# Kernel optimization log

Measured on AMD Instinct MI355X. Metric: run time of the kernel, lower is better.

Reference implementation:

```python
import jax, jax.numpy as jnp
import numpy as np

B, N, W, H = 2, 2048, 1024, 16
HD = W // H  # head dim = 64
STD = 0.02


def setup_inputs() -> dict:
    key = jax.random.key(0)
    ks = jax.random.split(key, 8)
    x = jax.random.normal(ks[0], (B, N, W), dtype=jnp.float32)
    # weights stored [in, out] (transposed vs torch nn.Linear)
    qkv_w = jax.random.normal(ks[1], (W, 3 * W), dtype=jnp.float32) * STD
    qkv_b = jnp.zeros((3 * W,), jnp.float32)
    proj_w = jax.random.normal(ks[2], (W, W), dtype=jnp.float32) * STD
    proj_b = jnp.zeros((W,), jnp.float32)
    fc_w = jax.random.normal(ks[3], (W, 4 * W), dtype=jnp.float32) * STD
    fc_b = jnp.zeros((4 * W,), jnp.float32)
    fc2_w = jax.random.normal(ks[4], (4 * W, W), dtype=jnp.float32) * STD
    fc2_b = jnp.zeros((W,), jnp.float32)
    ln1_g = jnp.ones((W,), jnp.float32)
    ln1_b = jnp.zeros((W,), jnp.float32)
    ln2_g = jnp.ones((W,), jnp.float32)
    ln2_b = jnp.zeros((W,), jnp.float32)
    return dict(x=x, ln1_g=ln1_g, ln1_b=ln1_b, qkv_w=qkv_w, qkv_b=qkv_b,
                proj_w=proj_w, proj_b=proj_b, ln2_g=ln2_g, ln2_b=ln2_b,
                fc_w=fc_w, fc_b=fc_b, fc2_w=fc2_w, fc2_b=fc2_b)


def _layernorm(x, g, b, eps=1e-5):
    mu = jnp.mean(x, axis=-1, keepdims=True)
    var = jnp.var(x, axis=-1, keepdims=True)
    return (x - mu) * jax.lax.rsqrt(var + eps) * g + b


def _attention(x, qkv_w, qkv_b, proj_w, proj_b):
    bs, n, w = x.shape
    qkv = x @ qkv_w + qkv_b                      # [b, n, 3W]
    qkv = qkv.reshape(bs, n, H, 3 * HD)
    q, k, v = jnp.split(qkv, 3, axis=-1)         # each [b, n, h, hd]
    scale = 1.0 / np.sqrt(np.sqrt(HD)).astype(np.float32)
    # hand-rolled attention: full [b, h, t, s] score matrix, fp32 softmax
    weight = jnp.einsum('bthc,bshc->bhts', q * scale, k * scale)
    weight = jax.nn.softmax(weight.astype(jnp.float32), axis=-1).astype(weight.dtype)
    out = jnp.einsum('bhts,bshc->bthc', weight, v).reshape(bs, n, w)
    return out @ proj_w + proj_b


def reference(x, ln1_g, ln1_b, qkv_w, qkv_b, proj_w, proj_b,
              ln2_g, ln2_b, fc_w, fc_b, fc2_w, fc2_b):
    x = x + _attention(_layernorm(x, ln1_g, ln1_b), qkv_w, qkv_b, proj_w, proj_b)
    h = _layernorm(x, ln2_g, ln2_b)
    h = jax.nn.gelu(h @ fc_w + fc_b, approximate=False) @ fc2_w + fc2_b
    return x + h
```

## Files before the change

### kernel.cpp

```cpp
#include <hip/hip_runtime.h>
#include <hip/hip_bf16.h>
#include <type_traits>
#include <cstdint>

using bf16 = __hip_bfloat16;
typedef __attribute__((ext_vector_type(8))) short bf16x8;
typedef __attribute__((ext_vector_type(4))) float f32x4;

__device__ __forceinline__ float bf2f(unsigned short u) {
    union { unsigned int i; float f; } c; c.i = ((unsigned int)u) << 16; return c.f;
}

#define GLLDS16(gp, lp)                                                          \
    __builtin_amdgcn_global_load_lds(                                            \
        (const __attribute__((address_space(1))) void*)(gp),                     \
        (__attribute__((address_space(3))) void*)(lp), 16, 0, 0)

__global__ __launch_bounds__(256) void transpose_f2b(const float* __restrict__ w,
                                                     bf16* __restrict__ wt,
                                                     int K, int N) {
    __shared__ bf16 t[32][33];
    const int tid = threadIdx.x;
    const int n0 = blockIdx.x * 32, k0 = blockIdx.y * 32;
#pragma unroll
    for (int i = 0; i < 4; ++i) {
        int idx = tid + i * 256;
        int r = idx >> 5, c = idx & 31;
        t[r][c] = __float2bfloat16(w[(size_t)(k0 + r) * N + n0 + c]);
    }
    __syncthreads();
#pragma unroll
    for (int i = 0; i < 4; ++i) {
        int idx = tid + i * 256;
        int r = idx >> 5, c = idx & 31;
        wt[(size_t)(n0 + r) * K + k0 + c] = t[c][r];
    }
}

__global__ __launch_bounds__(256) void vtrans_kernel(const bf16* __restrict__ qkv,
                                                     bf16* __restrict__ vtg) {
    __shared__ bf16 t[32][33];
    const int tid = threadIdx.x;
    const int s0 = blockIdx.x * 32, c0 = blockIdx.y * 32;
    const int bh = blockIdx.z, b = bh >> 4, h = bh & 15;
#pragma unroll
    for (int i = 0; i < 4; ++i) {
        int idx = tid + i * 256;
        int r = idx >> 5, c = idx & 31;
        t[r][c] = qkv[(size_t)(b * 2048 + s0 + r) * 3072 + h * 192 + 128 + c0 + c];
    }
    __syncthreads();
#pragma unroll
    for (int i = 0; i < 4; ++i) {
        int idx = tid + i * 256;
        int r = idx >> 5, c = idx & 31;
        vtg[((size_t)bh * 64 + c0 + r) * 2048 + s0 + c] = t[c][r];
    }
}

template <typename InT>
__global__ __launch_bounds__(256) void ln_kernel(const InT* __restrict__ x,
                                                 const float* __restrict__ g,
                                                 const float* __restrict__ bta,
                                                 bf16* __restrict__ y) {
    const int row = blockIdx.x, tid = threadIdx.x;
    const size_t base = (size_t)row * 1024 + tid * 4;
    float v[4];
    if constexpr (std::is_same_v<InT, float>) {
        float4 f = *(const float4*)(x + base);
        v[0] = f.x; v[1] = f.y; v[2] = f.z; v[3] = f.w;
    } else {
        ushort4 u = *(const ushort4*)((const unsigned short*)x + base);
        v[0] = bf2f(u.x); v[1] = bf2f(u.y); v[2] = bf2f(u.z); v[3] = bf2f(u.w);
    }
    float s = v[0] + v[1] + v[2] + v[3];
    float sq = v[0]*v[0] + v[1]*v[1] + v[2]*v[2] + v[3]*v[3];
#pragma unroll
    for (int off = 32; off > 0; off >>= 1) {
        s  += __shfl_down(s, off);
        sq += __shfl_down(sq, off);
    }
    __shared__ float red[8];
    const int wave = tid >> 6, lane = tid & 63;
    if (lane == 0) { red[wave] = s; red[4 + wave] = sq; }
    __syncthreads();
    s  = red[0] + red[1] + red[2] + red[3];
    sq = red[4] + red[5] + red[6] + red[7];
    const float mu   = s * (1.0f / 1024.0f);
    const float var  = sq * (1.0f / 1024.0f) - mu * mu;
    const float rstd = rsqrtf(var + 1e-5f);
#pragma unroll
    for (int e = 0; e < 4; ++e) {
        int col = tid * 4 + e;
        float yy = (v[e] - mu) * rstd * g[col] + bta[col];
        y[base + e] = __float2bfloat16(yy);
    }
}

template <int EPI, int BM>
__global__ __launch_bounds__(256) void gemm_kernel(const bf16* __restrict__ A,
                                                   const bf16* __restrict__ Bt,
                                                   const float* __restrict__ bias,
                                                   const void* __restrict__ resid,
                                                   void* __restrict__ Cout,
                                                   int M, int N, int K) {
    constexpr int IF = 4;
    constexpr int JF = (BM == 128) ? 4 : 2;
    __shared__ bf16 As[BM][72];
    __shared__ bf16 Bs[128][72];
    const int tid  = threadIdx.x;
    const int wave = tid >> 6, lane = tid & 63;
    const int quad = lane >> 4, l16 = lane & 15;
    const int wm = (BM == 128) ? (wave >> 1) * 64 : 0;
    const int wn = (BM == 128) ? (wave & 1) * 64 : wave * 32;
    const int bm = blockIdx.y * BM, bn = blockIdx.x * 128;

    int kz0 = 0, kz1 = K;
    if constexpr (EPI == 4) {
        kz0 = blockIdx.z * (K >> 1);
        kz1 = kz0 + (K >> 1);
    }

    f32x4 acc[IF][JF];
#pragma unroll
    for (int i = 0; i < IF; ++i)
#pragma unroll
        for (int j = 0; j < JF; ++j) acc[i][j] = (f32x4){0.f, 0.f, 0.f, 0.f};

    for (int kt = kz0; kt < kz1; kt += 64) {
        __syncthreads();
#pragma unroll
        for (int i = 0; i < BM * 8 / 256; ++i) {
            int c0 = tid + i * 256;
            int r = c0 >> 3, kc = (c0 & 7) << 3;
            *(uint4*)(&As[r][kc]) = *(const uint4*)(A + (size_t)(bm + r) * K + kt + kc);
        }
#pragma unroll
        for (int i = 0; i < 4; ++i) {
            int c0 = tid + i * 256;
            int r = c0 >> 3, kc = (c0 & 7) << 3;
            *(uint4*)(&Bs[r][kc]) = *(const uint4*)(Bt + (size_t)(bn + r) * K + kt + kc);
        }
        __syncthreads();
#pragma unroll
        for (int ks = 0; ks < 2; ++ks) {
            bf16x8 af[IF], bfr[JF];
#pragma unroll
            for (int i = 0; i < IF; ++i)
                af[i] = *(const bf16x8*)(&As[wm + i * 16 + l16][ks * 32 + quad * 8]);
#pragma unroll
            for (int j = 0; j < JF; ++j)
                bfr[j] = *(const bf16x8*)(&Bs[wn + j * 16 + l16][ks * 32 + quad * 8]);
#pragma unroll
            for (int i = 0; i < IF; ++i)
#pragma unroll
                for (int j = 0; j < JF; ++j)
                    acc[i][j] = __builtin_amdgcn_mfma_f32_16x16x32_bf16(af[i], bfr[j], acc[i][j], 0, 0, 0);
        }
    }
    float* skdst = nullptr;
    if constexpr (EPI == 4)
        skdst = blockIdx.z ? (float*)const_cast<void*>(resid) : (float*)Cout;
#pragma unroll
    for (int i = 0; i < IF; ++i) {
#pragma unroll
        for (int j = 0; j < JF; ++j) {
#pragma unroll
            for (int r = 0; r < 4; ++r) {
                const int row = bm + wm + i * 16 + quad * 4 + r;
                const int col = bn + wn + j * 16 + l16;
                float v = acc[i][j][r];
                if constexpr (EPI != 4) v += bias[col];
                if constexpr (EPI == 1)
                    v = 0.5f * v * (1.0f + erff(v * 0.70710678118654752f));
                if constexpr (EPI == 2) {
                    v += ((const float*)resid)[(size_t)row * N + col];
                    ((bf16*)Cout)[(size_t)row * N + col] = __float2bfloat16(v);
                } else if constexpr (EPI == 3) {
                    v += bf2f(((const unsigned short*)resid)[(size_t)row * N + col]);
                    ((float*)Cout)[(size_t)row * N + col] = v;
                } else if constexpr (EPI == 4) {
                    skdst[(size_t)row * N + col] = v;
                } else {
                    ((bf16*)Cout)[(size_t)row * N + col] = __float2bfloat16(v);
                }
            }
        }
    }
}

__global__ __launch_bounds__(256) void merge_fc2(const float* __restrict__ p0,
                                                 const float* __restrict__ p1,
                                                 const float* __restrict__ bias,
                                                 const bf16* __restrict__ resid,
                                                 float* __restrict__ outp) {
    const int idx = blockIdx.x * 256 + threadIdx.x;
    const int row = idx >> 8, col = (idx & 255) * 4;
    const size_t off = (size_t)row * 1024 + col;
    float4 a = *(const float4*)(p0 + off);
    float4 b = *(const float4*)(p1 + off);
    float4 bs = *(const float4*)(bias + col);
    ushort4 r = *(const ushort4*)((const unsigned short*)resid + off);
    float4 o;
    o.x = a.x + b.x + bs.x + bf2f(r.x);
    o.y = a.y + b.y + bs.y + bf2f(r.y);
    o.z = a.z + b.z + bs.z + bf2f(r.z);
    o.w = a.w + b.w + bs.w + bf2f(r.w);
    *(float4*)(outp + off) = o;
}

__global__ __launch_bounds__(256) void attn_kernel(const bf16* __restrict__ qkv,
                                                   const bf16* __restrict__ vtg,
                                                   bf16* __restrict__ Opart,
                                                   float* __restrict__ Lp) {
    __shared__ __align__(16) bf16 Ks[64 * 64];
    __shared__ __align__(16) bf16 Vs[64 * 64];
    __shared__ __align__(16) bf16 Ps[4][2][16][72];
    const int tid  = threadIdx.x;
    const int wave = tid >> 6, lane = tid & 63;
    const int quad = lane >> 4, l16 = lane & 15;
    const int qt = blockIdx.x, h = blockIdx.y;
    const int b = blockIdx.z >> 1, seg = blockIdx.z & 1;
    const size_t tok0 = (size_t)b * 2048;
    const int qbase = qt * 128 + wave * 32;

    bf16x8 qf[2][2];
#pragma unroll
    for (int set = 0; set < 2; ++set) {
        const bf16* qp = qkv + (tok0 + qbase + set * 16 + l16) * 3072 + h * 192 + quad * 8;
        qf[set][0] = *(const bf16x8*)(qp);
        qf[set][1] = *(const bf16x8*)(qp + 32);
    }

    const int swc = ((tid & 7) ^ ((tid >> 3) & 7)) * 8;
    const bf16* kg = qkv + (tok0 + (tid >> 3)) * 3072 + h * 192 + 64 + swc;
    const bf16* vg = vtg + ((size_t)(b * 16 + h) * 64 + (tid >> 3)) * 2048 + swc;

    const short oneb = 0x3f80;
    const bf16x8 ones = {oneb, oneb, oneb, oneb, oneb, oneb, oneb, oneb};

    f32x4 o[2][4], l_acc[2];
#pragma unroll
    for (int set = 0; set < 2; ++set) {
        l_acc[set] = (f32x4){0.f, 0.f, 0.f, 0.f};
#pragma unroll
        for (int j = 0; j < 4; ++j) o[set][j] = (f32x4){0.f, 0.f, 0.f, 0.f};
    }

    const int kt0 = seg * 1024;
    for (int kt = kt0; kt < kt0 + 1024; kt += 64) {
        __syncthreads();
        GLLDS16(kg + (size_t)kt * 3072,        &Ks[(wave * 64) * 8]);
        GLLDS16(kg + (size_t)(kt + 32) * 3072, &Ks[(wave * 64 + 256) * 8]);
        GLLDS16(vg + kt,                       &Vs[(wave * 64) * 8]);
        GLLDS16(vg + kt + 32 * 2048,           &Vs[(wave * 64 + 256) * 8]);
        __syncthreads();

#pragma unroll
        for (int j = 0; j < 4; ++j) {
            const int rk = j * 16 + l16;
            const int sw = l16 & 7;
            bf16x8 kb0 = *(const bf16x8*)(&Ks[rk * 64 + ((quad ^ sw) * 8)]);
            bf16x8 kb1 = *(const bf16x8*)(&Ks[rk * 64 + (((quad + 4) ^ sw) * 8)]);
#pragma unroll
            for (int set = 0; set < 2; ++set) {
                f32x4 s4 = (f32x4){0.f, 0.f, 0.f, 0.f};
                s4 = __builtin_amdgcn_mfma_f32_16x16x32_bf16(qf[set][0], kb0, s4, 0, 0, 0);
                s4 = __builtin_amdgcn_mfma_f32_16x16x32_bf16(qf[set][1], kb1, s4, 0, 0, 0);
#pragma unroll
                for (int r = 0; r < 4; ++r)
                    Ps[wave][set][quad * 4 + r][j * 16 + l16] =
                        __float2bfloat16(__expf(s4[r] * 0.125f));
            }
        }
#pragma unroll
        for (int kk = 0; kk < 2; ++kk) {
            bf16x8 pf0 = *(const bf16x8*)(&Ps[wave][0][l16][kk * 32 + quad * 8]);
            bf16x8 pf1 = *(const bf16x8*)(&Ps[wave][1][l16][kk * 32 + quad * 8]);
            l_acc[0] = __builtin_amdgcn_mfma_f32_16x16x32_bf16(pf0, ones, l_acc[0], 0, 0, 0);
            l_acc[1] = __builtin_amdgcn_mfma_f32_16x16x32_bf16(pf1, ones, l_acc[1], 0, 0, 0);
#pragma unroll
            for (int j = 0; j < 4; ++j) {
                const int rv = j * 16 + l16;
                bf16x8 vf = *(const bf16x8*)(&Vs[rv * 64 + (((kk * 4 + quad) ^ (l16 & 7)) * 8)]);
                o[0][j] = __builtin_amdgcn_mfma_f32_16x16x32_bf16(pf0, vf, o[0][j], 0, 0, 0);
                o[1][j] = __builtin_amdgcn_mfma_f32_16x16x32_bf16(pf1, vf, o[1][j], 0, 0, 0);
            }
        }
    }
    const size_t segoff = (size_t)seg * 4096;
#pragma unroll
    for (int set = 0; set < 2; ++set)
#pragma unroll
        for (int j = 0; j < 4; ++j)
#pragma unroll
            for (int r = 0; r < 4; ++r) {
                int row = qbase + set * 16 + quad * 4 + r;
                Opart[(segoff + tok0 + row) * 1024 + h * 64 + j * 16 + l16] =
                    __float2bfloat16(o[set][j][r]);
            }
    if (l16 == 0) {
#pragma unroll
        for (int set = 0; set < 2; ++set)
#pragma unroll
            for (int r = 0; r < 4; ++r) {
                int row = qbase + set * 16 + quad * 4 + r;
                Lp[(segoff + tok0 + row) * 16 + h] = l_acc[set][r];
            }
    }
}

__global__ __launch_bounds__(256) void merge_kernel(const bf16* __restrict__ Opart,
                                                    const float* __restrict__ Lp,
                                                    bf16* __restrict__ outp) {
    const int idx = blockIdx.x * 256 + threadIdx.x;
    const int c4 = idx & 15, h = (idx >> 4) & 15, gt = idx >> 8;
    const size_t li0 = (size_t)gt * 16 + h, li1 = li0 + 4096 * 16;
    float inv = 1.0f / (Lp[li0] + Lp[li1]);
    const size_t off = (size_t)gt * 1024 + h * 64 + c4 * 4;
    ushort4 a = *(const ushort4*)((const unsigned short*)Opart + off);
    ushort4 bb = *(const ushort4*)((const unsigned short*)Opart + off + (size_t)4096 * 1024);
    float va[4] = {bf2f(a.x), bf2f(a.y), bf2f(a.z), bf2f(a.w)};
    float vb[4] = {bf2f(bb.x), bf2f(bb.y), bf2f(bb.z), bf2f(bb.w)};
    unsigned short res[4];
#pragma unroll
    for (int e = 0; e < 4; ++e) {
        bf16 o = __float2bfloat16((va[e] + vb[e]) * inv);
        res[e] = *(unsigned short*)&o;
    }
    *(ushort4*)((unsigned short*)outp + off) = make_ushort4(res[0], res[1], res[2], res[3]);
}

extern "C" void kernel_launch(void* const* d_in, const int* in_sizes, int n_in,
                              void* d_out, int out_size, void* d_ws, size_t ws_size,
                              hipStream_t stream) {
    const float* x      = (const float*)d_in[0];
    const float* ln1_g  = (const float*)d_in[1];
    const float* ln1_b  = (const float*)d_in[2];
    const float* qkv_w  = (const float*)d_in[3];
    const float* qkv_b  = (const float*)d_in[4];
    const float* proj_w = (const float*)d_in[5];
    const float* proj_b = (const float*)d_in[6];
    const float* ln2_g  = (const float*)d_in[7];
    const float* ln2_b  = (const float*)d_in[8];
    const float* fc_w   = (const float*)d_in[9];
    const float* fc_b   = (const float*)d_in[10];
    const float* fc2_w  = (const float*)d_in[11];
    const float* fc2_b  = (const float*)d_in[12];
    float* outp = (float*)d_out;

    char* ws = (char*)d_ws;
    const size_t MB = 1024 * 1024;
    bf16*  wfcT   = (bf16*)(ws + 0 * MB);
    float* part1  = (float*)(ws + 0 * MB);
    bf16*  lnbuf  = (bf16*)(ws + 8 * MB);
    bf16*  wprojT = (bf16*)(ws + 8 * MB);
    float* Lp     = (float*)(ws + 10 * MB);
    bf16*  wqkvT  = (bf16*)(ws + 16 * MB);
    bf16*  vtg    = (bf16*)(ws + 16 * MB);
    bf16*  attnout= (bf16*)(ws + 16 * MB);
    bf16*  fcact  = (bf16*)(ws + 16 * MB);
    bf16*  qkvb   = (bf16*)(ws + 24 * MB);
    bf16*  Opart  = (bf16*)(ws + 48 * MB);
    bf16*  wfc2T  = (bf16*)(ws + 48 * MB);
    bf16*  x1     = (bf16*)(ws + 56 * MB);

    transpose_f2b<<<dim3(96, 32),  256, 0, stream>>>(qkv_w, wqkvT, 1024, 3072);
    transpose_f2b<<<dim3(128, 32), 256, 0, stream>>>(fc_w,  wfcT,  1024, 4096);
    ln_kernel<float><<<4096, 256, 0, stream>>>(x, ln1_g, ln1_b, lnbuf);
    gemm_kernel<0, 128><<<dim3(24, 32), 256, 0, stream>>>(lnbuf, wqkvT, qkv_b, nullptr, qkvb, 4096, 3072, 1024);
    vtrans_kernel<<<dim3(64, 2, 32), 256, 0, stream>>>(qkvb, vtg);
    transpose_f2b<<<dim3(32, 32), 256, 0, stream>>>(proj_w, wprojT, 1024, 1024);
    attn_kernel<<<dim3(16, 16, 4), 256, 0, stream>>>(qkvb, vtg, Opart, Lp);
    merge_kernel<<<4096, 256, 0, stream>>>(Opart, Lp, attnout);
    transpose_f2b<<<dim3(32, 128), 256, 0, stream>>>(fc2_w, wfc2T, 4096, 1024);
    gemm_kernel<2, 64><<<dim3(8, 64), 256, 0, stream>>>(attnout, wprojT, proj_b, x, x1, 4096, 1024, 1024);
    ln_kernel<bf16><<<4096, 256, 0, stream>>>(x1, ln2_g, ln2_b, lnbuf);
    gemm_kernel<1, 128><<<dim3(32, 32), 256, 0, stream>>>(lnbuf, wfcT, fc_b, nullptr, fcact, 4096, 4096, 1024);
    gemm_kernel<4, 64><<<dim3(8, 64, 2), 256, 0, stream>>>(fcact, wfc2T, nullptr, part1, outp, 4096, 1024, 4096);
    merge_fc2<<<4096, 256, 0, stream>>>(outp, part1, fc2_b, x1, outp);
}
```

Baseline: 388.4 us.

## Double-buffer GEMM tiles via direct global-to-LDS loads, swizzle blocks, approximate GELU

The GEMM kernel now stages A and B tiles into two XOR-swizzled LDS buffers with global_load_lds, loading the next K tile while the current one is computed. This replaces the register round-trip copies and halves the barriers per iteration. The proj and fc2 GEMMs also remap block indices across groups of eight, aimed at XCD/L2 locality. Exact erff in the GELU epilogue is swapped for an Abramowitz-Stegun polynomial using a hardware reciprocal, and the attention PV MFMA section raises wave priority. The polynomial GELU adds small approximation error, and the swizzle assumes the block count divides evenly by eight.

```diff
diff --git a/kernel.cpp b/kernel.cpp
--- a/kernel.cpp
+++ b/kernel.cpp
@@ -9,6 +9,17 @@
 
 __device__ __forceinline__ float bf2f(unsigned short u) {
     union { unsigned int i; float f; } c; c.i = ((unsigned int)u) << 16; return c.f;
+}
+
+__device__ __forceinline__ float gelu_f(float v) {
+    float x  = v * 0.70710678118654752f;
+    float ax = fabsf(x);
+    float t  = __builtin_amdgcn_rcpf(1.0f + 0.3275911f * ax);
+    float poly = ((((1.061405429f * t - 1.453152027f) * t + 1.421413741f) * t
+                   - 0.284496736f) * t + 0.254829592f) * t;
+    float erfv = 1.0f - poly * __expf(-ax * ax);
+    erfv = copysignf(erfv, x);
+    return 0.5f * v * (1.0f + erfv);
 }
 
 #define GLLDS16(gp, lp)                                                          \
@@ -97,7 +108,7 @@
     }
 }
 
-template <int EPI, int BM>
+template <int EPI, int BM, bool XSWZ>
 __global__ __launch_bounds__(256) void gemm_kernel(const bf16* __restrict__ A,
                                                    const bf16* __restrict__ Bt,
                                                    const float* __restrict__ bias,
@@ -106,61 +117,82 @@
                                                    int M, int N, int K) {
     constexpr int IF = 4;
     constexpr int JF = (BM == 128) ? 4 : 2;
-    __shared__ bf16 As[BM][72];
-    __shared__ bf16 Bs[128][72];
+    constexpr int AI = BM / 32;
+    __shared__ __align__(16) bf16 As[2][BM * 64];
+    __shared__ __align__(16) bf16 Bs[2][128 * 64];
     const int tid  = threadIdx.x;
     const int wave = tid >> 6, lane = tid & 63;
     const int quad = lane >> 4, l16 = lane & 15;
     const int wm = (BM == 128) ? (wave >> 1) * 64 : 0;
     const int wn = (BM == 128) ? (wave & 1) * 64 : wave * 32;
-    const int bm = blockIdx.y * BM, bn = blockIdx.x * 128;
+
+    int bx = blockIdx.x, by = blockIdx.y, bz = blockIdx.z;
+    if constexpr (XSWZ) {
+        const int gx = gridDim.x, gy = gridDim.y;
+        const int nwg = gx * gy * gridDim.z;
+        const int f = bx + gx * (by + gy * bz);
+        const int s = (f & 7) * (nwg >> 3) + (f >> 3);
+        bx = s % gx; int rem = s / gx; by = rem % gy; bz = rem / gy;
+    }
+    const int bm = by * BM, bn = bx * 128;
 
     int kz0 = 0, kz1 = K;
     if constexpr (EPI == 4) {
-        kz0 = blockIdx.z * (K >> 1);
+        kz0 = bz * (K >> 1);
         kz1 = kz0 + (K >> 1);
     }
 
+    const int r8 = lane >> 3, sc = lane & 7;
+    const bf16* ag = A  + (size_t)(bm + wave * 8 + r8) * K + ((sc ^ r8) << 3);
+    const bf16* bg = Bt + (size_t)(bn + wave * 8 + r8) * K + ((sc ^ r8) << 3);
+
     f32x4 acc[IF][JF];
 #pragma unroll
     for (int i = 0; i < IF; ++i)
 #pragma unroll
         for (int j = 0; j < JF; ++j) acc[i][j] = (f32x4){0.f, 0.f, 0.f, 0.f};
 
-    for (int kt = kz0; kt < kz1; kt += 64) {
-        __syncthreads();
-#pragma unroll
-        for (int i = 0; i < BM * 8 / 256; ++i) {
-            int c0 = tid + i * 256;
-            int r = c0 >> 3, kc = (c0 & 7) << 3;
-            *(uint4*)(&As[r][kc]) = *(const uint4*)(A + (size_t)(bm + r) * K + kt + kc);
-        }
-#pragma unroll
-        for (int i = 0; i < 4; ++i) {
-            int c0 = tid + i * 256;
-            int r = c0 >> 3, kc = (c0 & 7) << 3;
-            *(uint4*)(&Bs[r][kc]) = *(const uint4*)(Bt + (size_t)(bn + r) * K + kt + kc);
-        }
-        __syncthreads();
+    auto stage = [&](int buf, int kt) {
+#pragma unroll
+        for (int i = 0; i < AI; ++i)
+            GLLDS16(ag + (size_t)(i * 32) * K + kt, &As[buf][(wave * 8 + i * 32) * 64]);
+#pragma unroll
+        for (int i = 0; i < 4; ++i)
+            GLLDS16(bg + (size_t)(i * 32) * K + kt, &Bs[buf][(wave * 8 + i * 32) * 64]);
+    };
+    auto compute = [&](int buf) {
 #pragma unroll
         for (int ks = 0; ks < 2; ++ks) {
             bf16x8 af[IF], bfr[JF];
+            const int swr = l16 & 7;
 #pragma unroll
             for (int i = 0; i < IF; ++i)
-                af[i] = *(const bf16x8*)(&As[wm + i * 16 + l16][ks * 32 + quad * 8]);
+                af[i] = *(const bf16x8*)(&As[buf][(wm + i * 16 + l16) * 64 +
+                                                  (((ks * 4 + quad) ^ swr) << 3)]);
 #pragma unroll
             for (int j = 0; j < JF; ++j)
-                bfr[j] = *(const bf16x8*)(&Bs[wn + j * 16 + l16][ks * 32 + quad * 8]);
+                bfr[j] = *(const bf16x8*)(&Bs[buf][(wn + j * 16 + l16) * 64 +
+                                                   (((ks * 4 + quad) ^ swr) << 3)]);
 #pragma unroll
             for (int i = 0; i < IF; ++i)
 #pragma unroll
                 for (int j = 0; j < JF; ++j)
                     acc[i][j] = __builtin_amdgcn_mfma_f32_16x16x32_bf16(af[i], bfr[j], acc[i][j], 0, 0, 0);
         }
-    }
+    };
+    stage(0, kz0);
+    __syncthreads();
+    int cur = 0;
+    for (int kt = kz0; kt < kz1; kt += 64) {
+        if (kt + 64 < kz1) stage(cur ^ 1, kt + 64);
+        compute(cur);
+        __syncthreads();
+        cur ^= 1;
+    }
+
     float* skdst = nullptr;
     if constexpr (EPI == 4)
-        skdst = blockIdx.z ? (float*)const_cast<void*>(resid) : (float*)Cout;
+        skdst = bz ? (float*)const_cast<void*>(resid) : (float*)Cout;
 #pragma unroll
     for (int i = 0; i < IF; ++i) {
 #pragma unroll
@@ -172,7 +204,7 @@
                 float v = acc[i][j][r];
                 if constexpr (EPI != 4) v += bias[col];
                 if constexpr (EPI == 1)
-                    v = 0.5f * v * (1.0f + erff(v * 0.70710678118654752f));
+                    v = gelu_f(v);
                 if constexpr (EPI == 2) {
                     v += ((const float*)resid)[(size_t)row * N + col];
                     ((bf16*)Cout)[(size_t)row * N + col] = __float2bfloat16(v);
@@ -273,6 +305,7 @@
                         __float2bfloat16(__expf(s4[r] * 0.125f));
             }
         }
+        __builtin_amdgcn_s_setprio(1);
 #pragma unroll
         for (int kk = 0; kk < 2; ++kk) {
             bf16x8 pf0 = *(const bf16x8*)(&Ps[wave][0][l16][kk * 32 + quad * 8]);
@@ -287,6 +320,7 @@
                 o[1][j] = __builtin_amdgcn_mfma_f32_16x16x32_bf16(pf1, vf, o[1][j], 0, 0, 0);
             }
         }
+        __builtin_amdgcn_s_setprio(0);
     }
     const size_t segoff = (size_t)seg * 4096;
 #pragma unroll
@@ -368,15 +402,15 @@
     transpose_f2b<<<dim3(96, 32),  256, 0, stream>>>(qkv_w, wqkvT, 1024, 3072);
     transpose_f2b<<<dim3(128, 32), 256, 0, stream>>>(fc_w,  wfcT,  1024, 4096);
     ln_kernel<float><<<4096, 256, 0, stream>>>(x, ln1_g, ln1_b, lnbuf);
-    gemm_kernel<0, 128><<<dim3(24, 32), 256, 0, stream>>>(lnbuf, wqkvT, qkv_b, nullptr, qkvb, 4096, 3072, 1024);
+    gemm_kernel<0, 128, false><<<dim3(24, 32), 256, 0, stream>>>(lnbuf, wqkvT, qkv_b, nullptr, qkvb, 4096, 3072, 1024);
     vtrans_kernel<<<dim3(64, 2, 32), 256, 0, stream>>>(qkvb, vtg);
     transpose_f2b<<<dim3(32, 32), 256, 0, stream>>>(proj_w, wprojT, 1024, 1024);
     attn_kernel<<<dim3(16, 16, 4), 256, 0, stream>>>(qkvb, vtg, Opart, Lp);
     merge_kernel<<<4096, 256, 0, stream>>>(Opart, Lp, attnout);
     transpose_f2b<<<dim3(32, 128), 256, 0, stream>>>(fc2_w, wfc2T, 4096, 1024);
-    gemm_kernel<2, 64><<<dim3(8, 64), 256, 0, stream>>>(attnout, wprojT, proj_b, x, x1, 4096, 1024, 1024);
+    gemm_kernel<2, 64, true><<<dim3(8, 64), 256, 0, stream>>>(attnout, wprojT, proj_b, x, x1, 4096, 1024, 1024);
     ln_kernel<bf16><<<4096, 256, 0, stream>>>(x1, ln2_g, ln2_b, lnbuf);
-    gemm_kernel<1, 128><<<dim3(32, 32), 256, 0, stream>>>(lnbuf, wfcT, fc_b, nullptr, fcact, 4096, 4096, 1024);
-    gemm_kernel<4, 64><<<dim3(8, 64, 2), 256, 0, stream>>>(fcact, wfc2T, nullptr, part1, outp, 4096, 1024, 4096);
+    gemm_kernel<1, 128, false><<<dim3(32, 32), 256, 0, stream>>>(lnbuf, wfcT, fc_b, nullptr, fcact, 4096, 4096, 1024);
+    gemm_kernel<4, 64, true><<<dim3(8, 64, 2), 256, 0, stream>>>(fcact, wfc2T, nullptr, part1, outp, 4096, 1024, 4096);
     merge_fc2<<<4096, 256, 0, stream>>>(outp, part1, fc2_b, x1, outp);
 }
```

Result: no change. 383.0 us (-1.4%).
